# Performance work log

Hardware: AMD Instinct MI355X
Metric: run time of the kernel (lower is better)

Reference implementation:

```python
import jax, jax.numpy as jnp
import numpy as np

B, IMG, P, D, HEADS, DEPTH = 8, 384, 16, 768, 12, 12
HD = D // HEADS  # 64
EPS = 1e-5


def _ln(x, s, b):
    m = x.mean(-1, keepdims=True)
    v = ((x - m) ** 2).mean(-1, keepdims=True)
    return (x - m) / jnp.sqrt(v + EPS) * s + b


def _rotate_half(x):
    x1, x2 = jnp.split(x, 2, axis=-1)
    return jnp.concatenate([-x2, x1], axis=-1)


def _build_2d_rope(gh, gw, hd):
    half = hd // 2
    inv_freq = 1.0 / (10000.0 ** (jnp.arange(0, half, 2, dtype=jnp.float32) / half))  # [hd//4]
    yf = jnp.arange(gh, dtype=jnp.float32)[:, None] * inv_freq[None, :]  # [gh, hd//4]
    xf = jnp.arange(gw, dtype=jnp.float32)[:, None] * inv_freq[None, :]  # [gw, hd//4]
    yf = jnp.broadcast_to(yf[:, None, :], (gh, gw, half // 2))
    xf = jnp.broadcast_to(xf[None, :, :], (gh, gw, half // 2))
    comb = jnp.concatenate([yf, xf], axis=-1)          # [gh, gw, hd//2]
    comb = jnp.repeat(comb, 2, axis=-1)                # [gh, gw, hd]
    return jnp.sin(comb).reshape(-1, hd), jnp.cos(comb).reshape(-1, hd)


def _forward(x, patch_w, patch_b, cls_token, ln1_s, ln1_b, qkv_w, proj_w, proj_b,
             ln2_s, ln2_b, mlp_w1, mlp_b1, mlp_w2, mlp_b2, norm_s, norm_b):
    Bb, _, H, W = x.shape
    gh, gw = H // P, W // P
    # patch embed: Conv2d(3, D, P, stride=P) == reshape to patches + matmul
    patches = x.reshape(Bb, 3, gh, P, gw, P).transpose(0, 2, 4, 1, 3, 5).reshape(Bb, gh * gw, 3 * P * P)
    t = patches @ patch_w.reshape(D, -1).T + patch_b  # [B, L0, D]
    sin, cos = _build_2d_rope(gh, gw, HD)             # [L0, HD]
    t = jnp.concatenate([jnp.broadcast_to(cls_token, (Bb, 1, D)), t], axis=1)  # [B, L, D]
    L = t.shape[1]
    scale = HD ** -0.5
    sin_b = sin[None, None]  # [1,1,L0,HD]
    cos_b = cos[None, None]

    def rope(u):
        return u * cos_b + _rotate_half(u) * sin_b

    for i in range(DEPTH):
        h = _ln(t, ln1_s[i], ln1_b[i])
        qkv = (h @ qkv_w[i].T).reshape(Bb, L, 3, HEADS, HD).transpose(2, 0, 3, 1, 4)
        q, k, v = qkv[0], qkv[1], qkv[2]  # [B, H, L, HD]
        # RoPE on patch tokens only (CLS token untouched)
        q = jnp.concatenate([q[:, :, :1], rope(q[:, :, 1:])], axis=2)
        k = jnp.concatenate([k[:, :, :1], rope(k[:, :, 1:])], axis=2)
        attn = jnp.einsum('bhqd,bhkd->bhqk', q, k) * scale
        attn = jax.nn.softmax(attn, axis=-1)
        o = jnp.einsum('bhqk,bhkd->bhqd', attn, v).transpose(0, 2, 1, 3).reshape(Bb, L, D)
        t = t + o @ proj_w[i].T + proj_b[i]
        h2 = _ln(t, ln2_s[i], ln2_b[i])
        t = t + jax.nn.gelu(h2 @ mlp_w1[i].T + mlp_b1[i], approximate=False) @ mlp_w2[i].T + mlp_b2[i]

    return _ln(t[:, 0], norm_s, norm_b)  # [B, D]


def setup_inputs() -> dict:
    key = jax.random.key(0)
    ks = jax.random.split(key, 8)
    s = 0.02
    HID = 4 * D
    return {
        'x': jax.random.normal(ks[0], (B, 3, IMG, IMG), jnp.float32),
        'patch_w': jax.random.normal(ks[1], (D, 3, P, P), jnp.float32) * s,
        'patch_b': jnp.zeros((D,), jnp.float32),
        'cls_token': jnp.zeros((1, 1, D), jnp.float32),
        'ln1_s': jnp.ones((DEPTH, D), jnp.float32),
        'ln1_b': jnp.zeros((DEPTH, D), jnp.float32),
        'qkv_w': jax.random.normal(ks[2], (DEPTH, 3 * D, D), jnp.float32) * s,
        'proj_w': jax.random.normal(ks[3], (DEPTH, D, D), jnp.float32) * s,
        'proj_b': jnp.zeros((DEPTH, D), jnp.float32),
        'ln2_s': jnp.ones((DEPTH, D), jnp.float32),
        'ln2_b': jnp.zeros((DEPTH, D), jnp.float32),
        'mlp_w1': jax.random.normal(ks[4], (DEPTH, HID, D), jnp.float32) * s,
        'mlp_b1': jnp.zeros((DEPTH, HID), jnp.float32),
        'mlp_w2': jax.random.normal(ks[5], (DEPTH, D, HID), jnp.float32) * s,
        'mlp_b2': jnp.zeros((DEPTH, D), jnp.float32),
        'norm_s': jnp.ones((D,), jnp.float32),
        'norm_b': jnp.zeros((D,), jnp.float32),
    }


def reference(x, patch_w, patch_b, cls_token, ln1_s, ln1_b, qkv_w, proj_w, proj_b,
              ln2_s, ln2_b, mlp_w1, mlp_b1, mlp_w2, mlp_b2, norm_s, norm_b):
    return _forward(x, patch_w, patch_b, cls_token, ln1_s, ln1_b, qkv_w, proj_w, proj_b,
                    ln2_s, ln2_b, mlp_w1, mlp_b1, mlp_w2, mlp_b2, norm_s, norm_b)
```

## Files before the change

### kernel.cpp

```cpp
#include <hip/hip_runtime.h>
#include <math.h>

#define NB 8
#define DDIM 768
#define NHEAD 12
#define NDEPTH 12
#define HDIM 64
#define GRIDW 24
#define NL0 576
#define NL 577
#define LPAD 640
#define NHID 3072
#define MROWS (NB*NL)
#define MPAD 4736
#define EPSV 1e-5f
#define QTILES 10
#define NCONV 512

typedef unsigned short ushortT;
typedef __attribute__((ext_vector_type(8))) short bf16x8;
typedef __attribute__((ext_vector_type(4))) float f32x4;

__device__ __forceinline__ ushortT f2b(float f) {
    union { float f; unsigned u; } x; x.f = f;
    unsigned r = x.u + 0x7fffu + ((x.u >> 16) & 1u);
    return (ushortT)(r >> 16);
}

__device__ __forceinline__ float b2f(ushortT u) {
    union { unsigned u; float f; } x; x.u = ((unsigned)u) << 16;
    return x.f;
}

__device__ __forceinline__ void load_lds16(const void* g, void* l) {
    __builtin_amdgcn_global_load_lds((const __attribute__((address_space(1))) void*)g,
                                     (__attribute__((address_space(3))) void*)l, 16, 0, 0);
}

__global__ void f2b_k(const float* __restrict__ in, ushortT* __restrict__ out, long n) {
    for (long i = ((long)blockIdx.x * 256 + threadIdx.x) * 4; i < n; i += (long)gridDim.x * 1024) {
        float4 v = *(const float4*)(in + i);
        ushort4 o; o.x = f2b(v.x); o.y = f2b(v.y); o.z = f2b(v.z); o.w = f2b(v.w);
        *(ushort4*)(out + i) = o;
    }
}

__global__ void wconv4_k(const float* __restrict__ a, ushortT* __restrict__ ao, long na,
                         const float* __restrict__ b, ushortT* __restrict__ bo, long nb,
                         const float* __restrict__ c, ushortT* __restrict__ co, long nc,
                         const float* __restrict__ d, ushortT* __restrict__ dd, long nd) {
    long stride = (long)gridDim.x * 1024;
    long i0 = ((long)blockIdx.x * 256 + threadIdx.x) * 4;
    for (long i = i0; i < na; i += stride) {
        float4 v = *(const float4*)(a + i);
        ushort4 o; o.x = f2b(v.x); o.y = f2b(v.y); o.z = f2b(v.z); o.w = f2b(v.w);
        *(ushort4*)(ao + i) = o;
    }
    for (long i = i0; i < nb; i += stride) {
        float4 v = *(const float4*)(b + i);
        ushort4 o; o.x = f2b(v.x); o.y = f2b(v.y); o.z = f2b(v.z); o.w = f2b(v.w);
        *(ushort4*)(bo + i) = o;
    }
    for (long i = i0; i < nc; i += stride) {
        float4 v = *(const float4*)(c + i);
        ushort4 o; o.x = f2b(v.x); o.y = f2b(v.y); o.z = f2b(v.z); o.w = f2b(v.w);
        *(ushort4*)(co + i) = o;
    }
    for (long i = i0; i < nd; i += stride) {
        float4 v = *(const float4*)(d + i);
        ushort4 o; o.x = f2b(v.x); o.y = f2b(v.y); o.z = f2b(v.z); o.w = f2b(v.w);
        *(ushort4*)(dd + i) = o;
    }
}

__global__ void im2col_k(const float* __restrict__ x, ushortT* __restrict__ p) {
    for (long idx = (long)blockIdx.x * 256 + threadIdx.x; idx < (long)4608 * 768; idx += (long)gridDim.x * 256) {
        int row = (int)(idx / 768), col = (int)(idx - (long)row * 768);
        int b = row / NL0, pi = row - b * NL0;
        int gy = pi / GRIDW, gx = pi - gy * GRIDW;
        int c = col >> 8, r = col & 255;
        int py = r >> 4, px = r & 15;
        p[idx] = f2b(x[(((long)(b * 3 + c) * 384) + gy * 16 + py) * 384 + gx * 16 + px]);
    }
}

__global__ void cls_k(const float* __restrict__ cls, float* __restrict__ t) {
    t[(long)blockIdx.x * NL * DDIM + threadIdx.x] = cls[threadIdx.x];
}

__global__ void rope_k(float* __restrict__ sin_t, float* __restrict__ cos_t) {
    int pos = blockIdx.x, d = threadIdx.x;
    int gy = pos / GRIDW, gx = pos - gy * GRIDW;
    int j = d >> 1;
    float ang;
    if (j < 16) ang = (float)gy * powf(10000.f, -(float)j / 16.f);
    else        ang = (float)gx * powf(10000.f, -(float)(j - 16) / 16.f);
    sin_t[pos * 64 + d] = sinf(ang);
    cos_t[pos * 64 + d] = cosf(ang);
}

__global__ __launch_bounds__(256) void ln_k(const float* __restrict__ in,
                                            const float* __restrict__ sc,
                                            const float* __restrict__ bi,
                                            float* __restrict__ outf,
                                            ushortT* __restrict__ outb,
                                            long in_rstride) {
    int row = blockIdx.x;
    const float* ip = in + (long)row * in_rstride;
    float x[3];
    float s = 0.f, s2 = 0.f;
    #pragma unroll
    for (int i = 0; i < 3; ++i) {
        x[i] = ip[threadIdx.x + i * 256];
        s += x[i]; s2 += x[i] * x[i];
    }
    __shared__ float red0[256], red1[256];
    red0[threadIdx.x] = s; red1[threadIdx.x] = s2;
    __syncthreads();
    for (int off = 128; off; off >>= 1) {
        if (threadIdx.x < off) {
            red0[threadIdx.x] += red0[threadIdx.x + off];
            red1[threadIdx.x] += red1[threadIdx.x + off];
        }
        __syncthreads();
    }
    float mean = red0[0] * (1.f / 768.f);
    float var  = red1[0] * (1.f / 768.f) - mean * mean;
    float inv = rsqrtf(var + EPSV);
    #pragma unroll
    for (int i = 0; i < 3; ++i) {
        int c = threadIdx.x + i * 256;
        float val = (x[i] - mean) * inv * sc[c] + bi[c];
        if (outb) outb[(long)row * 768 + c] = f2b(val);
        else      outf[(long)row * 768 + c] = val;
    }
}

__global__ __launch_bounds__(256) void red_ln_k(const ushortT* __restrict__ psum,
                                                const float* __restrict__ b2,
                                                float* __restrict__ t,
                                                const float* __restrict__ sc,
                                                const float* __restrict__ bi,
                                                ushortT* __restrict__ outb) {
    int row = blockIdx.x;
    const size_t S = (size_t)MPAD * DDIM;
    const size_t rb = (size_t)row * DDIM;
    float x[3];
    float s = 0.f, s2 = 0.f;
    #pragma unroll
    for (int i = 0; i < 3; ++i) {
        int c = threadIdx.x + i * 256;
        float v = t[rb + c] + b2[c] + b2f(psum[rb + c]) + b2f(psum[S + rb + c])
                + b2f(psum[2 * S + rb + c]) + b2f(psum[3 * S + rb + c]);
        x[i] = v; s += v; s2 += v * v;
        t[rb + c] = v;
    }
    __shared__ float red0[256], red1[256];
    red0[threadIdx.x] = s; red1[threadIdx.x] = s2;
    __syncthreads();
    for (int off = 128; off; off >>= 1) {
        if (threadIdx.x < off) {
            red0[threadIdx.x] += red0[threadIdx.x + off];
            red1[threadIdx.x] += red1[threadIdx.x + off];
        }
        __syncthreads();
    }
    float mean = red0[0] * (1.f / 768.f);
    float var  = red1[0] * (1.f / 768.f) - mean * mean;
    float inv = rsqrtf(var + EPSV);
    #pragma unroll
    for (int i = 0; i < 3; ++i) {
        int c = threadIdx.x + i * 256;
        outb[rb + c] = f2b((x[i] - mean) * inv * sc[c] + bi[c]);
    }
}

__global__ __launch_bounds__(256) void red_final_k(const ushortT* __restrict__ psum,
                                                   const float* __restrict__ b2,
                                                   const float* __restrict__ t,
                                                   const float* __restrict__ sc,
                                                   const float* __restrict__ bi,
                                                   float* __restrict__ outf) {
    int row = blockIdx.x * NL;
    const size_t S = (size_t)MPAD * DDIM;
    const size_t rb = (size_t)row * DDIM;
    float x[3];
    float s = 0.f, s2 = 0.f;
    #pragma unroll
    for (int i = 0; i < 3; ++i) {
        int c = threadIdx.x + i * 256;
        float v = t[rb + c] + b2[c] + b2f(psum[rb + c]) + b2f(psum[S + rb + c])
                + b2f(psum[2 * S + rb + c]) + b2f(psum[3 * S + rb + c]);
        x[i] = v; s += v; s2 += v * v;
    }
    __shared__ float red0[256], red1[256];
    red0[threadIdx.x] = s; red1[threadIdx.x] = s2;
    __syncthreads();
    for (int off = 128; off; off >>= 1) {
        if (threadIdx.x < off) {
            red0[threadIdx.x] += red0[threadIdx.x + off];
            red1[threadIdx.x] += red1[threadIdx.x + off];
        }
        __syncthreads();
    }
    float mean = red0[0] * (1.f / 768.f);
    float var  = red1[0] * (1.f / 768.f) - mean * mean;
    float inv = rsqrtf(var + EPSV);
    #pragma unroll
    for (int i = 0; i < 3; ++i) {
        int c = threadIdx.x + i * 256;
        outf[(long)blockIdx.x * 768 + c] = (x[i] - mean) * inv * sc[c] + bi[c];
    }
}

template<int WR, int WC, int MI, int NI, int SPLITK, int NW>
__global__ __launch_bounds__(NW * 64) void gemm_t(const ushortT* __restrict__ A,
                                                  const ushortT* __restrict__ W,
                                                  const float* __restrict__ bias,
                                                  const float* __restrict__ resid,
                                                  float* __restrict__ Cf,
                                                  ushortT* __restrict__ Cb,
                                                  const float* __restrict__ sinT,
                                                  const float* __restrict__ cosT,
                                                  ushortT* __restrict__ qo,
                                                  ushortT* __restrict__ ko,
                                                  ushortT* __restrict__ vo,
                                                  ushortT* __restrict__ psum,
                                                  int N, int K, int flags) {
    constexpr int BM = WR * MI * 16;
    constexpr int BN = WC * NI * 16;
    constexpr int THREADS = NW * 64;
    constexpr int ACH = (BM * 64) / (THREADS * 8);
    constexpr int BCH = (BN * 64) / (THREADS * 8);
    __shared__ ushortT As[2][BM * 64];
    __shared__ ushortT Bs[2][BN * 64];
    int tid = threadIdx.x;
    int lane = tid & 63, wid = tid >> 6;
    int wm = wid / WC, wn = wid % WC;
    int lr = lane & 15, lk = lane >> 4;
    int nwg = gridDim.x * gridDim.y;
    int flat = blockIdx.y * gridDim.x + blockIdx.x;
    int qq = nwg >> 3, rr = nwg & 7;
    int xcd = flat & 7, idx = flat >> 3;
    int wg = (xcd < rr ? xcd * (qq + 1) : rr * (qq + 1) + (xcd - rr) * qq) + idx;
    int bx = wg % gridDim.x, by = wg / gridDim.x;
    int m0 = by * BM, n0 = bx * BN;
    int kspan = K / SPLITK;
    int k0 = (SPLITK > 1) ? blockIdx.z * kspan : 0;
    f32x4 acc[MI][NI] = {};

    auto stage = [&](int buf, int kt) {
        #pragma unroll
        for (int i = 0; i < ACH; ++i) {
            int ch = i * THREADS + tid;
            int r = ch >> 3, cb = (ch & 7) * 16;
            int cbs = cb ^ ((r & 7) << 4);
            load_lds16(A + (size_t)(m0 + r) * K + kt + (cbs >> 1), &As[buf][ch * 8]);
        }
        #pragma unroll
        for (int i = 0; i < BCH; ++i) {
            int ch = i * THREADS + tid;
            int r = ch >> 3, cb = (ch & 7) * 16;
            int cbs = cb ^ ((r & 7) << 4);
            load_lds16(W + (size_t)(n0 + r) * K + kt + (cbs >> 1), &Bs[buf][ch * 8]);
        }
    };

    stage(0, k0);
    asm volatile("s_waitcnt vmcnt(0)" ::: "memory");
    __builtin_amdgcn_s_barrier();
    int nk = kspan / 64;
    int cur = 0;
    for (int it = 0; it < nk; ++it) {
        if (it + 1 < nk) stage(cur ^ 1, k0 + (it + 1) * 64);
        #pragma unroll
        for (int ks = 0; ks < 2; ++ks) {
            bf16x8 aF[MI], bF[NI];
            #pragma unroll
            for (int mi = 0; mi < MI; ++mi) {
                int row = wm * MI * 16 + mi * 16 + lr;
                aF[mi] = *(const bf16x8*)((const char*)&As[cur][0] + row * 128 +
                                          ((ks * 64 + lk * 16) ^ ((row & 7) << 4)));
            }
            #pragma unroll
            for (int ni = 0; ni < NI; ++ni) {
                int row = wn * NI * 16 + ni * 16 + lr;
                bF[ni] = *(const bf16x8*)((const char*)&Bs[cur][0] + row * 128 +
                                          ((ks * 64 + lk * 16) ^ ((row & 7) << 4)));
            }
            #pragma unroll
            for (int mi = 0; mi < MI; ++mi)
                #pragma unroll
                for (int ni = 0; ni < NI; ++ni)
                    acc[mi][ni] = __builtin_amdgcn_mfma_f32_16x16x32_bf16(aF[mi], bF[ni], acc[mi][ni], 0, 0, 0);
        }
        asm volatile("s_waitcnt vmcnt(0)" ::: "memory");
        __builtin_amdgcn_s_barrier();
        cur ^= 1;
    }

    if (SPLITK > 1) {
        #pragma unroll
        for (int mi = 0; mi < MI; ++mi) {
            int rbase = m0 + wm * MI * 16 + mi * 16 + (lane >> 4) * 4;
            #pragma unroll
            for (int ni = 0; ni < NI; ++ni) {
                int c = n0 + wn * NI * 16 + ni * 16 + lr;
                #pragma unroll
                for (int r = 0; r < 4; ++r)
                    psum[((size_t)blockIdx.z * MPAD + rbase + r) * N + c] = f2b(acc[mi][ni][r]);
            }
        }
        return;
    }
    if (flags & 64) {
        if constexpr (NI == 4) {
            #pragma unroll
            for (int mi = 0; mi < MI; ++mi) {
                #pragma unroll
                for (int r = 0; r < 4; ++r) {
                    int row = m0 + wm * MI * 16 + mi * 16 + (lane >> 4) * 4 + r;
                    if (row >= MROWS) continue;
                    int b = row / NL, l = row - b * NL;
                    #pragma unroll
                    for (int ni = 0; ni < NI; ++ni) {
                        int c = n0 + wn * 64 + ni * 16 + lr;
                        float val = acc[mi][ni][r];
                        int sel = c / DDIM;
                        int cc = c - sel * DDIM;
                        int h = cc >> 6, d = cc & 63;
                        if (sel < 2 && l > 0) {
                            int pos = l - 1;
                            float cs = cosT[pos * 64 + d], sn = sinT[pos * 64 + d];
                            float partner = acc[mi][ni ^ 2][r];
                            float rh = (d < 32) ? -partner : partner;
                            val = val * cs + rh * sn;
                        }
                        int bh = b * NHEAD + h;
                        if (sel == 0)      qo[((long)bh * LPAD + l) * HDIM + d] = f2b(val * 0.125f);
                        else if (sel == 1) ko[((long)bh * LPAD + l) * HDIM + d] = f2b(val);
                        else               vo[((long)bh * HDIM + d) * LPAD + l] = f2b(val);
                    }
                }
            }
        }
        return;
    }
    #pragma unroll
    for (int mi = 0; mi < MI; ++mi) {
        int rbase = m0 + wm * MI * 16 + mi * 16 + (lane >> 4) * 4;
        #pragma unroll
        for (int ni = 0; ni < NI; ++ni) {
            int c = n0 + wn * NI * 16 + ni * 16 + lr;
            float bv = (flags & 1) ? bias[c] : 0.f;
            #pragma unroll
            for (int r = 0; r < 4; ++r) {
                int row = rbase + r;
                float val = acc[mi][ni][r] + bv;
                if (flags & 4) val = 0.5f * val * (1.f + erff(val * 0.70710678118654752f));
                long orow = row;
                if (flags & 8) orow = (long)(row / NL0) * NL + 1 + (row % NL0);
                if (flags & 2) val += resid[orow * (long)N + c];
                if (flags & 16) Cf[orow * (long)N + c] = val;
                if (flags & 32) Cb[orow * (long)N + c] = f2b(val);
            }
        }
    }
}

__global__ __launch_bounds__(256) void fattn_k(const ushortT* __restrict__ q,
                                               const ushortT* __restrict__ k,
                                               const ushortT* __restrict__ vt,
                                               ushortT* __restrict__ o,
                                               const float* __restrict__ wa, ushortT* __restrict__ wao, long na,
                                               const float* __restrict__ wb, ushortT* __restrict__ wbo, long nbn,
                                               const float* __restrict__ wc, ushortT* __restrict__ wco, long nc,
                                               const float* __restrict__ wd, ushortT* __restrict__ wdo, long nd) {
    if (blockIdx.x >= 96 * QTILES) {
        int cid = blockIdx.x - 96 * QTILES;
        long stride = (long)NCONV * 1024;
        long i0 = ((long)cid * 256 + threadIdx.x) * 4;
        for (long i = i0; i < na; i += stride) {
            float4 v = *(const float4*)(wa + i);
            ushort4 t4; t4.x = f2b(v.x); t4.y = f2b(v.y); t4.z = f2b(v.z); t4.w = f2b(v.w);
            *(ushort4*)(wao + i) = t4;
        }
        for (long i = i0; i < nbn; i += stride) {
            float4 v = *(const float4*)(wb + i);
            ushort4 t4; t4.x = f2b(v.x); t4.y = f2b(v.y); t4.z = f2b(v.z); t4.w = f2b(v.w);
            *(ushort4*)(wbo + i) = t4;
        }
        for (long i = i0; i < nc; i += stride) {
            float4 v = *(const float4*)(wc + i);
            ushort4 t4; t4.x = f2b(v.x); t4.y = f2b(v.y); t4.z = f2b(v.z); t4.w = f2b(v.w);
            *(ushort4*)(wco + i) = t4;
        }
        for (long i = i0; i < nd; i += stride) {
            float4 v = *(const float4*)(wd + i);
            ushort4 t4; t4.x = f2b(v.x); t4.y = f2b(v.y); t4.z = f2b(v.z); t4.w = f2b(v.w);
            *(ushort4*)(wdo + i) = t4;
        }
        return;
    }
    __shared__ ushortT Qs[4096], Ks[4096], Vs[4096], Ps[4096];
    int tid = threadIdx.x;
    int wave = tid >> 6, lane = tid & 63;
    int lr = lane & 15, lk = lane >> 4, g = lk;
    int bh = blockIdx.x / QTILES, qt = blockIdx.x % QTILES;
    int q0 = qt * 64;
    int b = bh / NHEAD, h = bh - b * NHEAD;
    int l8 = lane >> 3, c16 = lane & 7;
    int colsw = (c16 * 16) ^ ((l8 & 7) << 4);

    {
        const ushortT* src = q + ((long)bh * LPAD + q0) * HDIM;
        #pragma unroll
        for (int j = 0; j < 2; ++j) {
            int row = wave * 16 + j * 8 + l8;
            load_lds16(src + (long)row * HDIM + (colsw >> 1), Qs + wave * 1024 + j * 512);
        }
    }
    __syncthreads();
    bf16x8 qF[2];
    #pragma unroll
    for (int ks = 0; ks < 2; ++ks) {
        int row = wave * 16 + lr;
        qF[ks] = *(const bf16x8*)((const char*)Qs + row * 128 + ((ks * 64 + lk * 16) ^ ((lr & 7) << 4)));
    }
    f32x4 oa[4] = {};
    float m_r[4], l_r[4];
    #pragma unroll
    for (int r = 0; r < 4; ++r) { m_r[r] = -3e38f; l_r[r] = 0.f; }

    for (int t0 = 0; t0 < QTILES; ++t0) {
        int k0 = t0 * 64;
        __syncthreads();
        {
            const ushortT* srck = k + ((long)bh * LPAD + k0) * HDIM;
            const ushortT* srcv = vt + (long)bh * HDIM * LPAD + k0;
            #pragma unroll
            for (int j = 0; j < 2; ++j) {
                int row = wave * 16 + j * 8 + l8;
                load_lds16(srck + (long)row * HDIM + (colsw >> 1), Ks + wave * 1024 + j * 512);
                load_lds16(srcv + (long)row * LPAD + (colsw >> 1), Vs + wave * 1024 + j * 512);
            }
        }
        __syncthreads();
        f32x4 s[4] = {};
        #pragma unroll
        for (int ks = 0; ks < 2; ++ks) {
            #pragma unroll
            for (int kt = 0; kt < 4; ++kt) {
                int row = kt * 16 + lr;
                bf16x8 kF = *(const bf16x8*)((const char*)Ks + row * 128 + ((ks * 64 + lk * 16) ^ ((lr & 7) << 4)));
                s[kt] = __builtin_amdgcn_mfma_f32_16x16x32_bf16(qF[ks], kF, s[kt], 0, 0, 0);
            }
        }
        if (k0 + 63 > 576) {
            #pragma unroll
            for (int kt = 0; kt < 4; ++kt)
                if (k0 + kt * 16 + lr > 576) {
                    #pragma unroll
                    for (int r = 0; r < 4; ++r) s[kt][r] = -3e38f;
                }
        }
        float mx[4], al[4], rs[4];
        #pragma unroll
        for (int r = 0; r < 4; ++r)
            mx[r] = fmaxf(fmaxf(s[0][r], s[1][r]), fmaxf(s[2][r], s[3][r]));
        #pragma unroll
        for (int off = 1; off < 16; off <<= 1) {
            #pragma unroll
            for (int r = 0; r < 4; ++r) mx[r] = fmaxf(mx[r], __shfl_xor(mx[r], off));
        }
        #pragma unroll
        for (int r = 0; r < 4; ++r) {
            float mn = fmaxf(m_r[r], mx[r]);
            al[r] = __expf(m_r[r] - mn);
            m_r[r] = mn;
            rs[r] = 0.f;
        }
        #pragma unroll
        for (int kt = 0; kt < 4; ++kt) {
            #pragma unroll
            for (int r = 0; r < 4; ++r) {
                float p = __expf(s[kt][r] - m_r[r]);
                rs[r] += p;
                int rowp = g * 4 + r;
                *(ushortT*)((char*)Ps + wave * 2048 + rowp * 128 +
                            ((kt * 32 + lr * 2) ^ ((rowp & 7) << 4))) = f2b(p);
            }
        }
        #pragma unroll
        for (int off = 1; off < 16; off <<= 1) {
            #pragma unroll
            for (int r = 0; r < 4; ++r) rs[r] += __shfl_xor(rs[r], off);
        }
        #pragma unroll
        for (int r = 0; r < 4; ++r) l_r[r] = l_r[r] * al[r] + rs[r];
        #pragma unroll
        for (int dt = 0; dt < 4; ++dt) {
            #pragma unroll
            for (int r = 0; r < 4; ++r) oa[dt][r] *= al[r];
        }
        __syncthreads();
        #pragma unroll
        for (int ks = 0; ks < 2; ++ks) {
            bf16x8 pA = *(const bf16x8*)((const char*)Ps + wave * 2048 + lr * 128 +
                                         ((ks * 64 + lk * 16) ^ ((lr & 7) << 4)));
            #pragma unroll
            for (int dt = 0; dt < 4; ++dt) {
                bf16x8 vF = *(const bf16x8*)((const char*)Vs + (dt * 16 + lr) * 128 +
                                             ((ks * 64 + lk * 16) ^ ((lr & 7) << 4)));
                oa[dt] = __builtin_amdgcn_mfma_f32_16x16x32_bf16(pA, vF, oa[dt], 0, 0, 0);
            }
        }
    }
    #pragma unroll
    for (int r = 0; r < 4; ++r) {
        int l = q0 + wave * 16 + g * 4 + r;
        if (l > 576) continue;
        float inv = 1.f / l_r[r];
        #pragma unroll
        for (int dt = 0; dt < 4; ++dt)
            o[((long)(b * NL + l)) * DDIM + h * HDIM + dt * 16 + lr] = f2b(oa[dt][r] * inv);
    }
}

extern "C" void kernel_launch(void* const* d_in, const int* in_sizes, int n_in,
                              void* d_out, int out_size, void* d_ws, size_t ws_size,
                              hipStream_t stream) {
    const float* x       = (const float*)d_in[0];
    const float* patch_w = (const float*)d_in[1];
    const float* patch_b = (const float*)d_in[2];
    const float* cls     = (const float*)d_in[3];
    const float* ln1_s   = (const float*)d_in[4];
    const float* ln1_b   = (const float*)d_in[5];
    const float* qkv_w   = (const float*)d_in[6];
    const float* proj_w  = (const float*)d_in[7];
    const float* proj_b  = (const float*)d_in[8];
    const float* ln2_s   = (const float*)d_in[9];
    const float* ln2_b   = (const float*)d_in[10];
    const float* mlp_w1  = (const float*)d_in[11];
    const float* mlp_b1  = (const float*)d_in[12];
    const float* mlp_w2  = (const float*)d_in[13];
    const float* mlp_b2  = (const float*)d_in[14];
    const float* norm_s  = (const float*)d_in[15];
    const float* norm_b  = (const float*)d_in[16];

    const size_t SZ_WQ = (size_t)3 * DDIM * DDIM;
    const size_t SZ_WP = (size_t)DDIM * DDIM;
    const size_t SZ_W1 = (size_t)NHID * DDIM;
    const size_t SZ_W2 = (size_t)DDIM * NHID;

    char* w = (char*)d_ws;
    float* t      = (float*)w;  w += (size_t)MPAD * DDIM * 4;
    float* sin_t  = (float*)w;  w += (size_t)NL0 * HDIM * 4;
    float* cos_t  = (float*)w;  w += (size_t)NL0 * HDIM * 4;
    ushortT* psum = (ushortT*)w; w += (size_t)4 * MPAD * DDIM * 2;
    ushortT* h_bf   = (ushortT*)w; w += (size_t)MPAD * DDIM * 2;
    ushortT* o_bf   = (ushortT*)w; w += (size_t)MPAD * DDIM * 2;
    ushortT* mlp_bf = (ushortT*)w; w += (size_t)MPAD * NHID * 2;
    ushortT* patches = mlp_bf;
    ushortT* q_bf   = (ushortT*)w; w += (size_t)96 * LPAD * HDIM * 2;
    ushortT* k_bf   = (ushortT*)w; w += (size_t)96 * LPAD * HDIM * 2;
    ushortT* v_t    = (ushortT*)w; w += (size_t)96 * HDIM * LPAD * 2;
    ushortT* pw_bf  = (ushortT*)w; w += (size_t)DDIM * 768 * 2;
    ushortT* wqB[2]; ushortT* wpB[2]; ushortT* w1B[2]; ushortT* w2B[2];
    for (int s = 0; s < 2; ++s) {
        wqB[s] = (ushortT*)w; w += SZ_WQ * 2;
        wpB[s] = (ushortT*)w; w += SZ_WP * 2;
        w1B[s] = (ushortT*)w; w += SZ_W1 * 2;
        w2B[s] = (ushortT*)w; w += SZ_W2 * 2;
    }

    const float* nfp = nullptr;
    ushortT* nus = nullptr;
    float* nf = nullptr;

    hipLaunchKernelGGL(rope_k, dim3(NL0), dim3(64), 0, stream, sin_t, cos_t);
    hipLaunchKernelGGL(im2col_k, dim3(2048), dim3(256), 0, stream, x, patches);
    hipLaunchKernelGGL(f2b_k, dim3(512), dim3(256), 0, stream, patch_w, pw_bf, (long)DDIM * 768);
    hipLaunchKernelGGL(cls_k, dim3(NB), dim3(DDIM), 0, stream, cls, t);
    hipLaunchKernelGGL(wconv4_k, dim3(1024), dim3(256), 0, stream,
                       qkv_w, wqB[0], (long)SZ_WQ,
                       proj_w, wpB[0], (long)SZ_WP,
                       mlp_w1, w1B[0], (long)SZ_W1,
                       mlp_w2, w2B[0], (long)SZ_W2);
    hipLaunchKernelGGL((gemm_t<1, 4, 4, 2, 1, 4>), dim3(DDIM / 128, 4608 / 64), dim3(256), 0, stream,
                       patches, pw_bf, patch_b, nfp, t, nus, nfp, nfp, nus, nus, nus, nus,
                       DDIM, 768, 1 | 8 | 16);

    for (int i = 0; i < NDEPTH; ++i) {
        int cur = i & 1, nxt = (i + 1) & 1;
        if (i == 0) {
            hipLaunchKernelGGL(ln_k, dim3(MROWS), dim3(256), 0, stream,
                               t, ln1_s, ln1_b, nf, h_bf, (long)DDIM);
        } else {
            hipLaunchKernelGGL(red_ln_k, dim3(MROWS), dim3(256), 0, stream,
                               psum, mlp_b2 + (i - 1) * DDIM, t,
                               ln1_s + i * DDIM, ln1_b + i * DDIM, h_bf);
        }
        hipLaunchKernelGGL((gemm_t<4, 2, 2, 4, 1, 8>), dim3((3 * DDIM) / 128, MPAD / 128), dim3(512), 0, stream,
                           h_bf, wqB[cur], nfp, nfp, nf, nus, sin_t, cos_t,
                           q_bf, k_bf, v_t, nus, 3 * DDIM, DDIM, 64);
        long cn = (i + 1 < NDEPTH) ? 1 : 0;
        hipLaunchKernelGGL(fattn_k, dim3(96 * QTILES + NCONV), dim3(256), 0, stream,
                           q_bf, k_bf, v_t, o_bf,
                           qkv_w + SZ_WQ * (i + 1), wqB[nxt], cn * (long)SZ_WQ,
                           proj_w + SZ_WP * (i + 1), wpB[nxt], cn * (long)SZ_WP,
                           mlp_w1 + SZ_W1 * (i + 1), w1B[nxt], cn * (long)SZ_W1,
                           mlp_w2 + SZ_W2 * (i + 1), w2B[nxt], cn * (long)SZ_W2);
        hipLaunchKernelGGL((gemm_t<1, 4, 4, 2, 1, 4>), dim3(DDIM / 128, MPAD / 64), dim3(256), 0, stream,
                           o_bf, wpB[cur], proj_b + i * DDIM, t, t, nus, nfp, nfp, nus, nus, nus, nus,
                           DDIM, DDIM, 1 | 2 | 16);
        hipLaunchKernelGGL(ln_k, dim3(MROWS), dim3(256), 0, stream,
                           t, ln2_s + i * DDIM, ln2_b + i * DDIM, nf, h_bf, (long)DDIM);
        hipLaunchKernelGGL((gemm_t<4, 2, 2, 4, 1, 8>), dim3(NHID / 128, MPAD / 128), dim3(512), 0, stream,
                           h_bf, w1B[cur], mlp_b1 + i * NHID, nfp, nf, mlp_bf, nfp, nfp,
                           nus, nus, nus, nus, NHID, DDIM, 1 | 4 | 32);
        hipLaunchKernelGGL((gemm_t<4, 2, 2, 4, 4, 8>), dim3(DDIM / 128, MPAD / 128, 4), dim3(512), 0, stream,
                           mlp_bf, w2B[cur], nfp, nfp, nf, nus, nfp, nfp,
                           nus, nus, nus, psum, DDIM, NHID, 0);
    }
    hipLaunchKernelGGL(red_final_k, dim3(NB), dim3(256), 0, stream,
                       psum, mlp_b2 + (NDEPTH - 1) * DDIM, t, norm_s, norm_b, (float*)d_out);
}
```

Before: 2.519 ms.

## Process two query tiles per attention block and retune proj/patch GEMM config

Each flash-attention block now handles 128 query rows as two 64-row sub-tiles sharing every K/V tile loaded into LDS. This halves K/V global traffic and block count, and drops the block-wide barrier before the PV product, since each wave's P region is private. The proj and patch-embed GEMMs switch to a different template configuration with 512 threads. Risks are higher register pressure from doubled accumulators, and fewer attention blocks leaving the GPU less occupied.

```diff
diff --git a/kernel.cpp b/kernel.cpp
--- a/kernel.cpp
+++ b/kernel.cpp
@@ -14,7 +14,7 @@
 #define MROWS (NB*NL)
 #define MPAD 4736
 #define EPSV 1e-5f
-#define QTILES 10
+#define QT2 5
 #define NCONV 512
 
 typedef unsigned short ushortT;
@@ -376,8 +376,8 @@
                                                const float* __restrict__ wb, ushortT* __restrict__ wbo, long nbn,
                                                const float* __restrict__ wc, ushortT* __restrict__ wco, long nc,
                                                const float* __restrict__ wd, ushortT* __restrict__ wdo, long nd) {
-    if (blockIdx.x >= 96 * QTILES) {
-        int cid = blockIdx.x - 96 * QTILES;
+    if (blockIdx.x >= 96 * QT2) {
+        int cid = blockIdx.x - 96 * QT2;
         long stride = (long)NCONV * 1024;
         long i0 = ((long)cid * 256 + threadIdx.x) * 4;
         for (long i = i0; i < na; i += stride) {
@@ -402,37 +402,43 @@
         }
         return;
     }
-    __shared__ ushortT Qs[4096], Ks[4096], Vs[4096], Ps[4096];
+    __shared__ ushortT Qs[2][4096], Ks[4096], Vs[4096], Ps[4096];
     int tid = threadIdx.x;
     int wave = tid >> 6, lane = tid & 63;
     int lr = lane & 15, lk = lane >> 4, g = lk;
-    int bh = blockIdx.x / QTILES, qt = blockIdx.x % QTILES;
-    int q0 = qt * 64;
+    int bh = blockIdx.x / QT2, qp = blockIdx.x % QT2;
+    int q0 = qp * 128;
     int b = bh / NHEAD, h = bh - b * NHEAD;
     int l8 = lane >> 3, c16 = lane & 7;
     int colsw = (c16 * 16) ^ ((l8 & 7) << 4);
 
-    {
-        const ushortT* src = q + ((long)bh * LPAD + q0) * HDIM;
+    #pragma unroll
+    for (int qs = 0; qs < 2; ++qs) {
+        const ushortT* src = q + ((long)bh * LPAD + q0 + qs * 64) * HDIM;
         #pragma unroll
         for (int j = 0; j < 2; ++j) {
             int row = wave * 16 + j * 8 + l8;
-            load_lds16(src + (long)row * HDIM + (colsw >> 1), Qs + wave * 1024 + j * 512);
+            load_lds16(src + (long)row * HDIM + (colsw >> 1), Qs[qs] + wave * 1024 + j * 512);
         }
     }
     __syncthreads();
-    bf16x8 qF[2];
-    #pragma unroll
-    for (int ks = 0; ks < 2; ++ks) {
-        int row = wave * 16 + lr;
-        qF[ks] = *(const bf16x8*)((const char*)Qs + row * 128 + ((ks * 64 + lk * 16) ^ ((lr & 7) << 4)));
-    }
-    f32x4 oa[4] = {};
-    float m_r[4], l_r[4];
-    #pragma unroll
-    for (int r = 0; r < 4; ++r) { m_r[r] = -3e38f; l_r[r] = 0.f; }
-
-    for (int t0 = 0; t0 < QTILES; ++t0) {
+    bf16x8 qF[2][2];
+    #pragma unroll
+    for (int qs = 0; qs < 2; ++qs)
+        #pragma unroll
+        for (int ks = 0; ks < 2; ++ks) {
+            int row = wave * 16 + lr;
+            qF[qs][ks] = *(const bf16x8*)((const char*)Qs[qs] + row * 128 +
+                                          ((ks * 64 + lk * 16) ^ ((lr & 7) << 4)));
+        }
+    f32x4 oa[2][4] = {};
+    float m_r[2][4], l_r[2][4];
+    #pragma unroll
+    for (int qs = 0; qs < 2; ++qs)
+        #pragma unroll
+        for (int r = 0; r < 4; ++r) { m_r[qs][r] = -3e38f; l_r[qs][r] = 0.f; }
+
+    for (int t0 = 0; t0 < 10; ++t0) {
         int k0 = t0 * 64;
         __syncthreads();
         {
@@ -446,84 +452,90 @@
             }
         }
         __syncthreads();
-        f32x4 s[4] = {};
-        #pragma unroll
-        for (int ks = 0; ks < 2; ++ks) {
+        #pragma unroll
+        for (int qs = 0; qs < 2; ++qs) {
+            f32x4 s[4] = {};
+            #pragma unroll
+            for (int ks = 0; ks < 2; ++ks) {
+                #pragma unroll
+                for (int kt = 0; kt < 4; ++kt) {
+                    int row = kt * 16 + lr;
+                    bf16x8 kF = *(const bf16x8*)((const char*)Ks + row * 128 +
+                                                 ((ks * 64 + lk * 16) ^ ((lr & 7) << 4)));
+                    s[kt] = __builtin_amdgcn_mfma_f32_16x16x32_bf16(qF[qs][ks], kF, s[kt], 0, 0, 0);
+                }
+            }
+            if (k0 + 63 > 576) {
+                #pragma unroll
+                for (int kt = 0; kt < 4; ++kt)
+                    if (k0 + kt * 16 + lr > 576) {
+                        #pragma unroll
+                        for (int r = 0; r < 4; ++r) s[kt][r] = -3e38f;
+                    }
+            }
+            float mx[4], al[4], rs[4];
+            #pragma unroll
+            for (int r = 0; r < 4; ++r)
+                mx[r] = fmaxf(fmaxf(s[0][r], s[1][r]), fmaxf(s[2][r], s[3][r]));
+            #pragma unroll
+            for (int off = 1; off < 16; off <<= 1) {
+                #pragma unroll
+                for (int r = 0; r < 4; ++r) mx[r] = fmaxf(mx[r], __shfl_xor(mx[r], off));
+            }
+            #pragma unroll
+            for (int r = 0; r < 4; ++r) {
+                float mn = fmaxf(m_r[qs][r], mx[r]);
+                al[r] = __expf(m_r[qs][r] - mn);
+                m_r[qs][r] = mn;
+                rs[r] = 0.f;
+            }
             #pragma unroll
             for (int kt = 0; kt < 4; ++kt) {
-                int row = kt * 16 + lr;
-                bf16x8 kF = *(const bf16x8*)((const char*)Ks + row * 128 + ((ks * 64 + lk * 16) ^ ((lr & 7) << 4)));
-                s[kt] = __builtin_amdgcn_mfma_f32_16x16x32_bf16(qF[ks], kF, s[kt], 0, 0, 0);
-            }
-        }
-        if (k0 + 63 > 576) {
-            #pragma unroll
-            for (int kt = 0; kt < 4; ++kt)
-                if (k0 + kt * 16 + lr > 576) {
-                    #pragma unroll
-                    for (int r = 0; r < 4; ++r) s[kt][r] = -3e38f;
+                #pragma unroll
+                for (int r = 0; r < 4; ++r) {
+                    float p = __expf(s[kt][r] - m_r[qs][r]);
+                    rs[r] += p;
+                    int rowp = g * 4 + r;
+                    *(ushortT*)((char*)Ps + wave * 2048 + rowp * 128 +
+                                ((kt * 32 + lr * 2) ^ ((rowp & 7) << 4))) = f2b(p);
                 }
-        }
-        float mx[4], al[4], rs[4];
-        #pragma unroll
-        for (int r = 0; r < 4; ++r)
-            mx[r] = fmaxf(fmaxf(s[0][r], s[1][r]), fmaxf(s[2][r], s[3][r]));
-        #pragma unroll
-        for (int off = 1; off < 16; off <<= 1) {
-            #pragma unroll
-            for (int r = 0; r < 4; ++r) mx[r] = fmaxf(mx[r], __shfl_xor(mx[r], off));
-        }
+            }
+            #pragma unroll
+            for (int off = 1; off < 16; off <<= 1) {
+                #pragma unroll
+                for (int r = 0; r < 4; ++r) rs[r] += __shfl_xor(rs[r], off);
+            }
+            #pragma unroll
+            for (int r = 0; r < 4; ++r) l_r[qs][r] = l_r[qs][r] * al[r] + rs[r];
+            #pragma unroll
+            for (int dt = 0; dt < 4; ++dt) {
+                #pragma unroll
+                for (int r = 0; r < 4; ++r) oa[qs][dt][r] *= al[r];
+            }
+            #pragma unroll
+            for (int ks = 0; ks < 2; ++ks) {
+                bf16x8 pA = *(const bf16x8*)((const char*)Ps + wave * 2048 + lr * 128 +
+                                             ((ks * 64 + lk * 16) ^ ((lr & 7) << 4)));
+                #pragma unroll
+                for (int dt = 0; dt < 4; ++dt) {
+                    bf16x8 vF = *(const bf16x8*)((const char*)Vs + (dt * 16 + lr) * 128 +
+                                                 ((ks * 64 + lk * 16) ^ ((lr & 7) << 4)));
+                    oa[qs][dt] = __builtin_amdgcn_mfma_f32_16x16x32_bf16(pA, vF, oa[qs][dt], 0, 0, 0);
+                }
+            }
+        }
+    }
+    #pragma unroll
+    for (int qs = 0; qs < 2; ++qs) {
         #pragma unroll
         for (int r = 0; r < 4; ++r) {
-            float mn = fmaxf(m_r[r], mx[r]);
-            al[r] = __expf(m_r[r] - mn);
-            m_r[r] = mn;
-            rs[r] = 0.f;
-        }
-        #pragma unroll
-        for (int kt = 0; kt < 4; ++kt) {
-            #pragma unroll
-            for (int r = 0; r < 4; ++r) {
-                float p = __expf(s[kt][r] - m_r[r]);
-                rs[r] += p;
-                int rowp = g * 4 + r;
-                *(ushortT*)((char*)Ps + wave * 2048 + rowp * 128 +
-                            ((kt * 32 + lr * 2) ^ ((rowp & 7) << 4))) = f2b(p);
-            }
-        }
-        #pragma unroll
-        for (int off = 1; off < 16; off <<= 1) {
-            #pragma unroll
-            for (int r = 0; r < 4; ++r) rs[r] += __shfl_xor(rs[r], off);
-        }
-        #pragma unroll
-        for (int r = 0; r < 4; ++r) l_r[r] = l_r[r] * al[r] + rs[r];
-        #pragma unroll
-        for (int dt = 0; dt < 4; ++dt) {
-            #pragma unroll
-            for (int r = 0; r < 4; ++r) oa[dt][r] *= al[r];
-        }
-        __syncthreads();
-        #pragma unroll
-        for (int ks = 0; ks < 2; ++ks) {
-            bf16x8 pA = *(const bf16x8*)((const char*)Ps + wave * 2048 + lr * 128 +
-                                         ((ks * 64 + lk * 16) ^ ((lr & 7) << 4)));
-            #pragma unroll
-            for (int dt = 0; dt < 4; ++dt) {
-                bf16x8 vF = *(const bf16x8*)((const char*)Vs + (dt * 16 + lr) * 128 +
-                                             ((ks * 64 + lk * 16) ^ ((lr & 7) << 4)));
-                oa[dt] = __builtin_amdgcn_mfma_f32_16x16x32_bf16(pA, vF, oa[dt], 0, 0, 0);
-            }
-        }
-    }
-    #pragma unroll
-    for (int r = 0; r < 4; ++r) {
-        int l = q0 + wave * 16 + g * 4 + r;
-        if (l > 576) continue;
-        float inv = 1.f / l_r[r];
-        #pragma unroll
-        for (int dt = 0; dt < 4; ++dt)
-            o[((long)(b * NL + l)) * DDIM + h * HDIM + dt * 16 + lr] = f2b(oa[dt][r] * inv);
+            int l = q0 + qs * 64 + wave * 16 + g * 4 + r;
+            if (l > 576) continue;
+            float inv = 1.f / l_r[qs][r];
+            #pragma unroll
+            for (int dt = 0; dt < 4; ++dt)
+                o[((long)(b * NL + l)) * DDIM + h * HDIM + dt * 16 + lr] = f2b(oa[qs][dt][r] * inv);
+        }
     }
 }
 
@@ -587,7 +599,7 @@
                        proj_w, wpB[0], (long)SZ_WP,
                        mlp_w1, w1B[0], (long)SZ_W1,
                        mlp_w2, w2B[0], (long)SZ_W2);
-    hipLaunchKernelGGL((gemm_t<1, 4, 4, 2, 1, 4>), dim3(DDIM / 128, 4608 / 64), dim3(256), 0, stream,
+    hipLaunchKernelGGL((gemm_t<2, 4, 2, 2, 1, 8>), dim3(DDIM / 128, 4608 / 64), dim3(512), 0, stream,
                        patches, pw_bf, patch_b, nfp, t, nus, nfp, nfp, nus, nus, nus, nus,
                        DDIM, 768, 1 | 8 | 16);
 
@@ -605,13 +617,13 @@
                            h_bf, wqB[cur], nfp, nfp, nf, nus, sin_t, cos_t,
                            q_bf, k_bf, v_t, nus, 3 * DDIM, DDIM, 64);
         long cn = (i + 1 < NDEPTH) ? 1 : 0;
-        hipLaunchKernelGGL(fattn_k, dim3(96 * QTILES + NCONV), dim3(256), 0, stream,
+        hipLaunchKernelGGL(fattn_k, dim3(96 * QT2 + NCONV), dim3(256), 0, stream,
                            q_bf, k_bf, v_t, o_bf,
                            qkv_w + SZ_WQ * (i + 1), wqB[nxt], cn * (long)SZ_WQ,
                            proj_w + SZ_WP * (i + 1), wpB[nxt], cn * (long)SZ_WP,
                            mlp_w1 + SZ_W1 * (i + 1), w1B[nxt], cn * (long)SZ_W1,
                            mlp_w2 + SZ_W2 * (i + 1), w2B[nxt], cn * (long)SZ_W2);
-        hipLaunchKernelGGL((gemm_t<1, 4, 4, 2, 1, 4>), dim3(DDIM / 128, MPAD / 64), dim3(256), 0, stream,
+        hipLaunchKernelGGL((gemm_t<2, 4, 2, 2, 1, 8>), dim3(DDIM / 128, MPAD / 64), dim3(512), 0, stream,
                            o_bf, wpB[cur], proj_b + i * DDIM, t, t, nus, nfp, nfp, nus, nus, nus, nus,
                            DDIM, DDIM, 1 | 2 | 16);
         hipLaunchKernelGGL(ln_k, dim3(MROWS), dim3(256), 0, stream,
```

Result: faster. 2.448 ms (-2.8%).
